# Kernel optimization log

Hardware: AMD Instinct MI355X
Metric: run time of the kernel (lower is better)

Reference implementation:

```python
import jax, jax.numpy as jnp
import numpy as np

NEG_SLOPE = 0.01  # torch F.leaky_relu default

def _lrelu(x):
    return jax.nn.leaky_relu(x, NEG_SLOPE)

def setup_inputs() -> dict:
    key = jax.random.key(0)
    ks = jax.random.split(key, 24)
    B, N, E = 512, 20000, 640000
    n_enc_1, n_enc_2, n_z = 512, 256, 64
    n_dec_2, n_dec_1, hidden = 256, 512, 256
    p = lambda k, shp, fan: jax.random.normal(k, shp, jnp.float32) * (1.0 / np.sqrt(fan))
    return {
        "data": jax.random.normal(ks[0], (B, N), jnp.float32),
        "noise": jax.random.normal(ks[1], (B, N), jnp.float32),
        "edge_index": jax.random.randint(ks[2], (2, E), 0, N, jnp.int32),
        "w_gcn": jax.random.normal(ks[3], (), jnp.float32),
        "b_gcn": jax.random.normal(ks[4], (), jnp.float32) * 0.1,
        "enc1_w": p(ks[5], (N, n_enc_1), N), "enc1_b": p(ks[6], (n_enc_1,), N),
        "enc2_w": p(ks[7], (n_enc_1, n_enc_2), n_enc_1), "enc2_b": p(ks[8], (n_enc_2,), n_enc_1),
        "enc3_w": p(ks[9], (n_enc_2, n_z), n_enc_2), "enc3_b": p(ks[10], (n_z,), n_enc_2),
        "dec1_w": p(ks[11], (n_z, n_dec_2), n_z), "dec1_b": p(ks[12], (n_dec_2,), n_z),
        "dec2_w": p(ks[13], (n_dec_2, n_dec_1), n_dec_2), "dec2_b": p(ks[14], (n_dec_1,), n_dec_2),
        "dec3_w": p(ks[15], (n_dec_1, N), n_dec_1), "dec3_b": p(ks[16], (N,), n_dec_1),
        "disc1_w": p(ks[17], (n_z, hidden), n_z), "disc1_b": p(ks[18], (hidden,), n_z),
        "disc2_w": p(ks[19], (hidden, hidden), hidden), "disc2_b": p(ks[20], (hidden,), hidden),
        "disc3_w": p(ks[21], (hidden, 1), hidden), "disc3_b": p(ks[22], (1,), hidden),
    }

def _gcn_batched(x, edge_index, w_gcn, b_gcn):
    # x: [B, N] -> GCNConv(1,1, improved=True) applied per row, vectorized.
    B, N = x.shape
    src, dst = edge_index[0], edge_index[1]
    loop = jnp.arange(N, dtype=src.dtype)
    src_a = jnp.concatenate([src, loop])
    dst_a = jnp.concatenate([dst, loop])
    # improved=True: self-loop edge weight 2.0
    ew = jnp.concatenate([jnp.ones(src.shape[0], x.dtype), jnp.full((N,), 2.0, x.dtype)])
    deg = jax.ops.segment_sum(ew, dst_a, num_segments=N)
    dinv = jnp.where(deg > 0, jax.lax.rsqrt(deg), 0.0)
    norm = dinv[src_a] * ew * dinv[dst_a]  # [E+N]
    xl = x * w_gcn                         # lin (1x1 weight, no bias)
    msgs = xl[:, src_a] * norm[None, :]    # [B, E+N]
    agg = jnp.zeros_like(x).at[:, dst_a].add(msgs)
    return agg + b_gcn

def reference(data, noise, edge_index, w_gcn, b_gcn,
              enc1_w, enc1_b, enc2_w, enc2_b, enc3_w, enc3_b,
              dec1_w, dec1_b, dec2_w, dec2_b, dec3_w, dec3_b,
              disc1_w, disc1_b, disc2_w, disc2_b, disc3_w, disc3_b):
    x = data + noise * 0.1
    gcn_out = _lrelu(_gcn_batched(x, edge_index, w_gcn, b_gcn))  # [B, N]
    h1 = _lrelu(gcn_out @ enc1_w + enc1_b)
    h2 = _lrelu(h1 @ enc2_w + enc2_b)
    z = _lrelu(h2 @ enc3_w + enc3_b)
    d1 = _lrelu(z @ dec1_w + dec1_b)
    d2 = _lrelu(d1 @ dec2_w + dec2_b)
    dec_h3 = _lrelu(d2 @ dec3_w + dec3_b)
    g1 = _lrelu(z @ disc1_w + disc1_b)
    g2 = _lrelu(g1 @ disc2_w + disc2_b)
    d = jax.nn.sigmoid(g2 @ disc3_w + disc3_b)
    return (dec_h3, z, d)
```

## Files before the change

### kernel.cpp

```cpp
#include <hip/hip_runtime.h>
#include <hip/hip_bf16.h>


#define LRELU(v) ((v) > 0.f ? (v) : 0.01f * (v))

static constexpr int Bb = 512;
static constexpr int Nn = 20000;
static constexpr int Ee = 640000;
static constexpr int KBn = 2500;
static constexpr int NPD = 20096;

typedef __attribute__((ext_vector_type(8))) short short8;
typedef __attribute__((ext_vector_type(4))) float f32x4;

__device__ __forceinline__ ushort f2bf(float f) {
  uint u = __builtin_bit_cast(uint, f);
  u = u + 0x7FFFu + ((u >> 16) & 1u);
  return (ushort)(u >> 16);
}
__device__ __forceinline__ float bfLo(uint u) {
  return __builtin_bit_cast(float, u << 16);
}
__device__ __forceinline__ float bfHi(uint u) {
  return __builtin_bit_cast(float, u & 0xffff0000u);
}

__global__ void transpose_xs_k(const float* __restrict__ a, const float* __restrict__ nz,
                               const float* __restrict__ dinv, ushort* __restrict__ xs) {
  __shared__ ushort tile[64][65];
  int c0 = blockIdx.x * 64;
  int p = blockIdx.y;
  int chunk = p >> 1;
  int sub = (p & 1) * 64;
  int rbase = p * 64;
  for (int i = threadIdx.x; i < 64 * 64; i += 256) {
    int rr = i >> 6, cc = i & 63;
    int r = rbase + rr, c = c0 + cc;
    ushort v = 0;
    if (c < Nn) {
      size_t idx = (size_t)r * Nn + c;
      v = f2bf(dinv[c] * (a[idx] + 0.1f * nz[idx]));
    }
    tile[rr][cc] = v;
  }
  __syncthreads();
  for (int i = threadIdx.x; i < 64 * 64; i += 256) {
    int cc = i >> 6, rr = i & 63;
    int c = c0 + cc;
    if (c < Nn) xs[(size_t)chunk * Nn * 128 + (size_t)c * 128 + sub + rr] = tile[rr][cc];
  }
}

__global__ void hist_check_k(const int* __restrict__ src, const int* __restrict__ dst, int E,
                             int* __restrict__ cnt, int* __restrict__ flag) {
  int i = blockIdx.x * 256 + threadIdx.x;
  if (i < E) {
    int s = src[i], d = dst[i];
    if ((unsigned)s >= (unsigned)Nn || (unsigned)d >= (unsigned)Nn) {
      atomicExch(flag, 1);
    } else {
      atomicAdd(&cnt[d], 1);
    }
  }
}

__global__ void offs_k(const int* __restrict__ cnt, int* __restrict__ offs,
                       int* __restrict__ cursor, float* __restrict__ dinv,
                       int* __restrict__ bump) {
  int i = blockIdx.x * 256 + threadIdx.x;
  int l = threadIdx.x & 63;
  int v = (i < Nn) ? cnt[i] : 0;
  int x = v;
#pragma unroll
  for (int d = 1; d < 64; d <<= 1) {
    int t = __shfl_up(x, d);
    if (l >= d) x += t;
  }
  int total = __shfl(x, 63);
  int base = 0;
  if (l == 0) base = atomicAdd(bump, total);
  base = __shfl(base, 0);
  int excl = base + x - v;
  if (i < Nn) {
    offs[i] = excl;
    cursor[i] = excl;
    dinv[i] = rsqrtf(2.0f + (float)v);
  }
}

__global__ void scatter_k(const int* __restrict__ src, const int* __restrict__ dst, int E,
                          int* __restrict__ cursor, uint* __restrict__ eOff) {
  int i = blockIdx.x * 256 + threadIdx.x;
  if (i < E) {
    int s = src[i], d = dst[i];
    if ((unsigned)s >= (unsigned)Nn || (unsigned)d >= (unsigned)Nn) return;
    int p = atomicAdd(&cursor[d], 1);
    eOff[p] = (uint)s * 256u;
  }
}

__global__ __launch_bounds__(256) void spmm_fm_k(
    const ushort* __restrict__ xs, const uint* __restrict__ eOff, const int* __restrict__ offs,
    const int* __restrict__ cnt, const float* __restrict__ dinv, const float* __restrict__ wg,
    const float* __restrict__ bg, ushort* __restrict__ gfm) {
  __shared__ uint sIdx[4][64];
  __shared__ ushort sOut[128][8];
  int bid = blockIdx.x;
  int chunk = bid & 3;
  int grp = bid >> 2;
  int wv = threadIdx.x >> 6, l = threadIdx.x & 63;
  const char* base = (const char*)(xs + (size_t)chunk * Nn * 128) + l * 4;
  float wgv = wg[0], bb = bg[0];

#pragma unroll
  for (int sub = 0; sub < 2; ++sub) {
    int n = grp * 8 + wv * 2 + sub;
    int o = offs[n], c = cnt[n];
    const uint* ep = eOff + o;
    uint su = *(const uint*)(base + (size_t)n * 256);
    float a00 = 2.0f * bfLo(su), a01 = 2.0f * bfHi(su);
    float a10 = 0.f, a11 = 0.f;

    for (int bi = 0; bi < c; bi += 64) {
      int rem = c - bi;
      if (rem > 64) rem = 64;
      sIdx[wv][l] = (l < rem) ? ep[bi + l] : 0u;
      int i = 0;
      for (; i + 16 <= rem; i += 16) {
        uint u[16];
#pragma unroll
        for (int j = 0; j < 16; ++j) u[j] = *(const uint*)(base + sIdx[wv][i + j]);
#pragma unroll
        for (int j = 0; j < 16; j += 2) {
          a00 += bfLo(u[j]);
          a01 += bfHi(u[j]);
          a10 += bfLo(u[j + 1]);
          a11 += bfHi(u[j + 1]);
        }
      }
      for (; i + 4 <= rem; i += 4) {
        uint u0 = *(const uint*)(base + sIdx[wv][i]);
        uint u1 = *(const uint*)(base + sIdx[wv][i + 1]);
        uint u2 = *(const uint*)(base + sIdx[wv][i + 2]);
        uint u3 = *(const uint*)(base + sIdx[wv][i + 3]);
        a00 += bfLo(u0);
        a01 += bfHi(u0);
        a10 += bfLo(u1);
        a11 += bfHi(u1);
        a00 += bfLo(u2);
        a01 += bfHi(u2);
        a10 += bfLo(u3);
        a11 += bfHi(u3);
      }
      for (; i < rem; ++i) {
        uint u = *(const uint*)(base + sIdx[wv][i]);
        a00 += bfLo(u);
        a01 += bfHi(u);
      }
    }

    float wdn = wgv * dinv[n];
    float v0 = wdn * (a00 + a10) + bb;
    float v1 = wdn * (a01 + a11) + bb;
    v0 = LRELU(v0);
    v1 = LRELU(v1);
    int j = wv * 2 + sub;
    sOut[2 * l][j] = f2bf(v0);
    sOut[2 * l + 1][j] = f2bf(v1);
  }
  __syncthreads();
  int row = threadIdx.x >> 1, half = threadIdx.x & 1;
  uint2 v = *(const uint2*)&sOut[row][half * 4];
  int m = chunk * 128 + row;
  *(uint2*)&gfm[((size_t)grp * 512 + m) * 8 + half * 4] = v;
}

__global__ void conv_we_k(const float* __restrict__ W, ushort* __restrict__ wef) {
  int n = blockIdx.x * 256 + threadIdx.x;
  int kb = blockIdx.y;
  ushort v[8];
#pragma unroll
  for (int j = 0; j < 8; ++j) v[j] = f2bf(W[(size_t)(8 * kb + j) * 512 + n]);
  uint4 pk;
  pk.x = (uint)v[0] | ((uint)v[1] << 16);
  pk.y = (uint)v[2] | ((uint)v[3] << 16);
  pk.z = (uint)v[4] | ((uint)v[5] << 16);
  pk.w = (uint)v[6] | ((uint)v[7] << 16);
  *(uint4*)&wef[((size_t)kb * 512 + n) * 8] = pk;
}

__global__ __launch_bounds__(256) void fmg_enc1_k(const ushort* __restrict__ gfm,
                                                  const ushort* __restrict__ wef,
                                                  float* __restrict__ C) {
  int n0 = blockIdx.x * 128, m0 = blockIdx.y * 128;
  int l = threadIdx.x & 63, w = threadIdx.x >> 6;
  int wr = w >> 1, wc = w & 1;
  int lrow = l & 15, lkg = l >> 4;
  f32x4 acc[4][4] = {};
  int ksBeg = blockIdx.z * 25, ksEnd = ksBeg + 25;

  for (int ks = ksBeg; ks < ksEnd; ++ks) {
    int kb = ks * 4 + lkg;
    short8 a[4], b[4];
#pragma unroll
    for (int mi = 0; mi < 4; ++mi) {
      int m = m0 + wr * 64 + mi * 16 + lrow;
      a[mi] = *(const short8*)&gfm[((size_t)kb * 512 + m) * 8];
    }
#pragma unroll
    for (int nj = 0; nj < 4; ++nj) {
      int n = n0 + wc * 64 + nj * 16 + lrow;
      b[nj] = *(const short8*)&wef[((size_t)kb * 512 + n) * 8];
    }
#pragma unroll
    for (int mi = 0; mi < 4; ++mi)
#pragma unroll
      for (int nj = 0; nj < 4; ++nj)
        acc[mi][nj] = __builtin_amdgcn_mfma_f32_16x16x32_bf16(a[mi], b[nj], acc[mi][nj], 0, 0, 0);
  }

#pragma unroll
  for (int mi = 0; mi < 4; ++mi)
#pragma unroll
    for (int nj = 0; nj < 4; ++nj)
#pragma unroll
      for (int r = 0; r < 4; ++r) {
        int row = m0 + wr * 64 + mi * 16 + lkg * 4 + r;
        int col = n0 + wc * 64 + nj * 16 + lrow;
        atomicAdd(&C[(size_t)row * 512 + col], acc[mi][nj][r]);
      }
}

__global__ void conv_wf_k(const float* __restrict__ W, ushort* __restrict__ wf) {
  int n = blockIdx.x * 256 + threadIdx.x;
  int kb = blockIdx.y;
  if (n >= NPD) return;
  ushort v[8];
#pragma unroll
  for (int j = 0; j < 8; ++j)
    v[j] = (n < Nn) ? f2bf(W[(size_t)(8 * kb + j) * Nn + n]) : (ushort)0;
  uint4 pk;
  pk.x = (uint)v[0] | ((uint)v[1] << 16);
  pk.y = (uint)v[2] | ((uint)v[3] << 16);
  pk.z = (uint)v[4] | ((uint)v[5] << 16);
  pk.w = (uint)v[6] | ((uint)v[7] << 16);
  *(uint4*)&wf[((size_t)kb * NPD + n) * 8] = pk;
}

__global__ __launch_bounds__(256) void fmg_dec3_k(const ushort* __restrict__ d2f,
                                                  const ushort* __restrict__ wf,
                                                  const float* __restrict__ bias,
                                                  float* __restrict__ C) {
  int n0 = blockIdx.x * 128, m0 = blockIdx.y * 128;
  int l = threadIdx.x & 63, w = threadIdx.x >> 6;
  int wr = w >> 1, wc = w & 1;
  int lrow = l & 15, lkg = l >> 4;
  f32x4 acc[4][4] = {};

#pragma unroll 4
  for (int ks = 0; ks < 16; ++ks) {
    int kb = ks * 4 + lkg;
    short8 a[4], b[4];
#pragma unroll
    for (int mi = 0; mi < 4; ++mi) {
      int m = m0 + wr * 64 + mi * 16 + lrow;
      a[mi] = *(const short8*)&d2f[((size_t)kb * 512 + m) * 8];
    }
#pragma unroll
    for (int nj = 0; nj < 4; ++nj) {
      int n = n0 + wc * 64 + nj * 16 + lrow;
      b[nj] = *(const short8*)&wf[((size_t)kb * NPD + n) * 8];
    }
#pragma unroll
    for (int mi = 0; mi < 4; ++mi)
#pragma unroll
      for (int nj = 0; nj < 4; ++nj)
        acc[mi][nj] = __builtin_amdgcn_mfma_f32_16x16x32_bf16(a[mi], b[nj], acc[mi][nj], 0, 0, 0);
  }

#pragma unroll
  for (int mi = 0; mi < 4; ++mi)
#pragma unroll
    for (int nj = 0; nj < 4; ++nj)
#pragma unroll
      for (int r = 0; r < 4; ++r) {
        int row = m0 + wr * 64 + mi * 16 + lkg * 4 + r;
        int col = n0 + wc * 64 + nj * 16 + lrow;
        if (col < Nn) {
          float v = acc[mi][nj][r] + bias[col];
          C[(size_t)row * Nn + col] = LRELU(v);
        }
      }
}

__global__ __launch_bounds__(256) void tailA_k(const float* __restrict__ h1,
                                               const float* __restrict__ c1,
                                               const float* __restrict__ W2,
                                               const float* __restrict__ c2,
                                               const float* __restrict__ W3,
                                               const float* __restrict__ c3,
                                               float* __restrict__ zbuf,
                                               float* __restrict__ out_z) {
  __shared__ float s_h1[512];
  __shared__ float s_h2[256];
  __shared__ float s_part[4][256];
  int rl = blockIdx.x;
  int t = threadIdx.x;
  int w = t >> 6, l = t & 63;

  {
    float r0 = h1[(size_t)rl * 512 + t] + c1[t];
    float r1 = h1[(size_t)rl * 512 + t + 256] + c1[t + 256];
    s_h1[t] = LRELU(r0);
    s_h1[t + 256] = LRELU(r1);
  }
  __syncthreads();

  {
    int c4 = l * 4;
    float a0 = 0.f, a1 = 0.f, a2 = 0.f, a3 = 0.f;
#pragma unroll 16
    for (int k = w * 128; k < w * 128 + 128; ++k) {
      float4 wv = *(const float4*)&W2[(size_t)k * 256 + c4];
      float x = s_h1[k];
      a0 += x * wv.x; a1 += x * wv.y; a2 += x * wv.z; a3 += x * wv.w;
    }
    float4 pv = {a0, a1, a2, a3};
    *(float4*)&s_part[w][c4] = pv;
  }
  __syncthreads();
  s_h2[t] = LRELU(s_part[0][t] + s_part[1][t] + s_part[2][t] + s_part[3][t] + c2[t]);
  __syncthreads();

  {
    int c = t >> 2, p = t & 3;
    float a = 0.f;
#pragma unroll 16
    for (int k = p * 64; k < p * 64 + 64; ++k) a += s_h2[k] * W3[(size_t)k * 64 + c];
    s_part[p][c] = a;
  }
  __syncthreads();
  if (t < 64) {
    float v = s_part[0][t] + s_part[1][t] + s_part[2][t] + s_part[3][t] + c3[t];
    v = LRELU(v);
    zbuf[(size_t)rl * 64 + t] = v;
    out_z[(size_t)rl * 64 + t] = v;
  }
}

__global__ __launch_bounds__(256) void tailB_k(
    const float* __restrict__ zbuf, const float* __restrict__ Wd1, const float* __restrict__ cd1,
    const float* __restrict__ Wd2, const float* __restrict__ cd2, const float* __restrict__ Wg1,
    const float* __restrict__ cg1, const float* __restrict__ Wg2, const float* __restrict__ cg2,
    const float* __restrict__ Wg3, const float* __restrict__ cg3, float* __restrict__ out_d,
    ushort* __restrict__ d2f) {
  __shared__ float s_z[64];
  __shared__ float s_x[256];
  __shared__ float s_part[4][256];
  __shared__ float s_g2[256];
  __shared__ float s_red[4];
  int bid = blockIdx.x;
  int rl = bid & 511;
  int t = threadIdx.x;
  int w = t >> 6, l = t & 63;

  if (t < 64) s_z[t] = zbuf[(size_t)rl * 64 + t];
  __syncthreads();

  if (bid < 512) {
    {
      float a = 0.f;
#pragma unroll
      for (int k = 0; k < 64; ++k) a += s_z[k] * Wd1[(size_t)k * 256 + t];
      s_x[t] = LRELU(a + cd1[t]);
    }
    __syncthreads();
    {
      int g = t & 127, p = t >> 7;
      int c4 = g * 4;
      float a0 = 0.f, a1 = 0.f, a2 = 0.f, a3 = 0.f;
#pragma unroll 16
      for (int k = p * 128; k < p * 128 + 128; ++k) {
        float4 wv = *(const float4*)&Wd2[(size_t)k * 512 + c4];
        float x = s_x[k];
        a0 += x * wv.x; a1 += x * wv.y; a2 += x * wv.z; a3 += x * wv.w;
      }
      float* sp = &s_part[0][0];
      float4 pv = {a0, a1, a2, a3};
      *(float4*)&sp[p * 512 + c4] = pv;
    }
    __syncthreads();
    {
      const float* sp = &s_part[0][0];
#pragma unroll
      for (int cc = 0; cc < 2; ++cc) {
        int c = t + cc * 256;
        float v = sp[c] + sp[512 + c] + cd2[c];
        v = LRELU(v);
        d2f[((size_t)(c >> 3) * 512 + rl) * 8 + (c & 7)] = f2bf(v);
      }
    }
  } else {
    {
      float a = 0.f;
#pragma unroll
      for (int k = 0; k < 64; ++k) a += s_z[k] * Wg1[(size_t)k * 256 + t];
      s_x[t] = LRELU(a + cg1[t]);
    }
    __syncthreads();
    {
      int c4 = l * 4;
      float a0 = 0.f, a1 = 0.f, a2 = 0.f, a3 = 0.f;
#pragma unroll 16
      for (int k = w * 64; k < w * 64 + 64; ++k) {
        float4 wv = *(const float4*)&Wg2[(size_t)k * 256 + c4];
        float x = s_x[k];
        a0 += x * wv.x; a1 += x * wv.y; a2 += x * wv.z; a3 += x * wv.w;
      }
      float4 pv = {a0, a1, a2, a3};
      *(float4*)&s_part[w][c4] = pv;
    }
    __syncthreads();
    s_g2[t] = LRELU(s_part[0][t] + s_part[1][t] + s_part[2][t] + s_part[3][t] + cg2[t]);
    __syncthreads();
    {
      float p = s_g2[t] * Wg3[t];
#pragma unroll
      for (int o = 32; o > 0; o >>= 1) p += __shfl_down(p, o);
      if ((t & 63) == 0) s_red[t >> 6] = p;
      __syncthreads();
      if (t == 0) {
        float s = s_red[0] + s_red[1] + s_red[2] + s_red[3] + cg3[0];
        out_d[rl] = 1.f / (1.f + __expf(-s));
      }
    }
  }
}

__global__ void sentinel_k(float* out, float val) { out[0] = val; }
__global__ void flag_sentinel_k(float* out, const int* flag) {
  if (*flag != 0) out[0] = 70000.0f;
}

extern "C" void kernel_launch(void* const* d_in, const int* in_sizes, int n_in,
                              void* d_out, int out_size, void* d_ws, size_t ws_size,
                              hipStream_t stream) {
  const float* data = (const float*)d_in[0];
  const float* noise = (const float*)d_in[1];
  const int* edge = (const int*)d_in[2];
  const int* esrc_in = edge;
  const int* edst_in = edge + Ee;
  const float* w_gcn = (const float*)d_in[3];
  const float* b_gcn = (const float*)d_in[4];
  const float* enc1_w = (const float*)d_in[5];
  const float* enc1_b = (const float*)d_in[6];
  const float* enc2_w = (const float*)d_in[7];
  const float* enc2_b = (const float*)d_in[8];
  const float* enc3_w = (const float*)d_in[9];
  const float* enc3_b = (const float*)d_in[10];
  const float* dec1_w = (const float*)d_in[11];
  const float* dec1_b = (const float*)d_in[12];
  const float* dec2_w = (const float*)d_in[13];
  const float* dec2_b = (const float*)d_in[14];
  const float* dec3_w = (const float*)d_in[15];
  const float* dec3_b = (const float*)d_in[16];
  const float* disc1_w = (const float*)d_in[17];
  const float* disc1_b = (const float*)d_in[18];
  const float* disc2_w = (const float*)d_in[19];
  const float* disc2_b = (const float*)d_in[20];
  const float* disc3_w = (const float*)d_in[21];
  const float* disc3_b = (const float*)d_in[22];

  char* w = (char*)d_ws;
  size_t o = 0;
  auto alloc = [&](size_t bytes) {
    size_t r = o;
    o = (o + bytes + 15) & ~(size_t)15;
    return r;
  };
  size_t r1 = alloc((size_t)64 * NPD * 8 * 2);
  ushort* xs = (ushort*)(w + r1);
  ushort* wef = (ushort*)(w + r1);
  ushort* wf = (ushort*)(w + r1);
  ushort* gfm = (ushort*)(w + alloc((size_t)KBn * 512 * 8 * 2));
  float* h1 = (float*)(w + alloc(512 * 512 * 4));
  ushort* d2f = (ushort*)(w + alloc((size_t)64 * 512 * 8 * 2));
  float* zbuf = (float*)(w + alloc((size_t)512 * 64 * 4));
  float* dinv = (float*)(w + alloc(Nn * 4));
  int* cnt = (int*)(w + alloc(Nn * 4));
  int* offs = (int*)(w + alloc(Nn * 4));
  int* cursor = (int*)(w + alloc(Nn * 4));
  uint* eOff = (uint*)(w + alloc(Ee * 4));
  int* flag = (int*)(w + alloc(16));

  float* outp = (float*)d_out;
  float* out_dec = outp;
  float* out_z = outp + (size_t)Bb * Nn;
  float* out_d = out_z + (size_t)Bb * 64;

  static const int expect_sizes[23] = {
      10240000, 10240000, 1280000, 1, 1,
      10240000, 512, 131072, 256, 16384, 64,
      16384, 256, 131072, 512, 10240000, 20000,
      16384, 256, 65536, 256, 256, 1};
  float host_sentinel = 0.f;
  if (n_in != 23) host_sentinel = 50000.f;
  else if (out_size != 10273280) host_sentinel = 80000.f;
  else if (ws_size < 46100000u) host_sentinel = 60000.f;
  else {
    for (int i = 0; i < 23; ++i)
      if (in_sizes[i] != expect_sizes[i]) { host_sentinel = 100000.f + 1000.f * i; break; }
  }

  hipMemsetAsync(cnt, 0, Nn * sizeof(int), stream);
  hipMemsetAsync(flag, 0, 2 * sizeof(int), stream);
  hipMemsetAsync(h1, 0, 512 * 512 * 4, stream);
  hist_check_k<<<(Ee + 255) / 256, 256, 0, stream>>>(esrc_in, edst_in, Ee, cnt, flag);
  offs_k<<<(Nn + 255) / 256, 256, 0, stream>>>(cnt, offs, cursor, dinv, flag + 1);
  scatter_k<<<(Ee + 255) / 256, 256, 0, stream>>>(esrc_in, edst_in, Ee, cursor, eOff);

  {
    dim3 g((Nn + 63) / 64, 8);
    transpose_xs_k<<<g, 256, 0, stream>>>(data, noise, dinv, xs);
  }
  spmm_fm_k<<<(Nn / 8) * 4, 256, 0, stream>>>(xs, eOff, offs, cnt, dinv, w_gcn, b_gcn, gfm);
  {
    dim3 g(2, KBn);
    conv_we_k<<<g, 256, 0, stream>>>(enc1_w, wef);
  }
  {
    dim3 g(512 / 128, 512 / 128, 25);
    fmg_enc1_k<<<g, 256, 0, stream>>>(gfm, wef, h1);
  }
  tailA_k<<<Bb, 256, 0, stream>>>(h1, enc1_b, enc2_w, enc2_b, enc3_w, enc3_b, zbuf, out_z);
  tailB_k<<<2 * Bb, 256, 0, stream>>>(zbuf, dec1_w, dec1_b, dec2_w, dec2_b, disc1_w, disc1_b,
                                      disc2_w, disc2_b, disc3_w, disc3_b, out_d, d2f);
  {
    dim3 g((NPD + 255) / 256, 64);
    conv_wf_k<<<g, 256, 0, stream>>>(dec3_w, wf);
  }
  {
    dim3 g(NPD / 128, 512 / 128);
    fmg_dec3_k<<<g, 256, 0, stream>>>(d2f, wf, dec3_b, out_dec);
  }

  flag_sentinel_k<<<1, 1, 0, stream>>>(out_dec, flag);
  if (host_sentinel != 0.f) sentinel_k<<<1, 1, 0, stream>>>(out_dec, host_sentinel);
}
```

Measured before the change: 284.5 us.

## Prefetch dec3 MFMA operands, widen enc1 split-K, vectorize SpMM index loads

The dec3 GEMM loop now software-prefetches the next K-step's A/B fragments into registers while issuing the current MFMAs, to hide global load latency. The enc1 split-K grid goes from 25 to 63 slices of 10 K-steps each, with a clamp on the last slice, to raise occupancy across CUs at the cost of more atomic or partial-sum traffic into h1. The SpMM gather reads shared-memory indices two at a time and separates index loads from data gathers to improve memory-level parallelism.

```diff
diff --git a/kernel.cpp b/kernel.cpp
--- a/kernel.cpp
+++ b/kernel.cpp
@@ -129,28 +129,37 @@
       for (; i + 16 <= rem; i += 16) {
         uint u[16];
 #pragma unroll
-        for (int j = 0; j < 16; ++j) u[j] = *(const uint*)(base + sIdx[wv][i + j]);
+        for (int j = 0; j < 8; ++j) {
+          uint2 pr = *(const uint2*)&sIdx[wv][i + 2 * j];
+          u[2 * j] = pr.x;
+          u[2 * j + 1] = pr.y;
+        }
+        uint g[16];
+#pragma unroll
+        for (int j = 0; j < 16; ++j) g[j] = *(const uint*)(base + u[j]);
 #pragma unroll
         for (int j = 0; j < 16; j += 2) {
-          a00 += bfLo(u[j]);
-          a01 += bfHi(u[j]);
-          a10 += bfLo(u[j + 1]);
-          a11 += bfHi(u[j + 1]);
+          a00 += bfLo(g[j]);
+          a01 += bfHi(g[j]);
+          a10 += bfLo(g[j + 1]);
+          a11 += bfHi(g[j + 1]);
         }
       }
       for (; i + 4 <= rem; i += 4) {
-        uint u0 = *(const uint*)(base + sIdx[wv][i]);
-        uint u1 = *(const uint*)(base + sIdx[wv][i + 1]);
-        uint u2 = *(const uint*)(base + sIdx[wv][i + 2]);
-        uint u3 = *(const uint*)(base + sIdx[wv][i + 3]);
-        a00 += bfLo(u0);
-        a01 += bfHi(u0);
-        a10 += bfLo(u1);
-        a11 += bfHi(u1);
-        a00 += bfLo(u2);
-        a01 += bfHi(u2);
-        a10 += bfLo(u3);
-        a11 += bfHi(u3);
+        uint2 p0 = *(const uint2*)&sIdx[wv][i];
+        uint2 p1 = *(const uint2*)&sIdx[wv][i + 2];
+        uint g0 = *(const uint*)(base + p0.x);
+        uint g1 = *(const uint*)(base + p0.y);
+        uint g2 = *(const uint*)(base + p1.x);
+        uint g3 = *(const uint*)(base + p1.y);
+        a00 += bfLo(g0);
+        a01 += bfHi(g0);
+        a10 += bfLo(g1);
+        a11 += bfHi(g1);
+        a00 += bfLo(g2);
+        a01 += bfHi(g2);
+        a10 += bfLo(g3);
+        a11 += bfHi(g3);
       }
       for (; i < rem; ++i) {
         uint u = *(const uint*)(base + sIdx[wv][i]);
@@ -197,7 +206,9 @@
   int wr = w >> 1, wc = w & 1;
   int lrow = l & 15, lkg = l >> 4;
   f32x4 acc[4][4] = {};
-  int ksBeg = blockIdx.z * 25, ksEnd = ksBeg + 25;
+  int ksBeg = blockIdx.z * 10;
+  int ksEnd = ksBeg + 10;
+  if (ksEnd > 625) ksEnd = 625;
 
   for (int ks = ksBeg; ks < ksEnd; ++ks) {
     int kb = ks * 4 + lkg;
@@ -257,26 +268,49 @@
   int lrow = l & 15, lkg = l >> 4;
   f32x4 acc[4][4] = {};
 
-#pragma unroll 4
+  int m_0 = m0 + wr * 64 + lrow, n_0 = n0 + wc * 64 + lrow;
+  short8 a0, a1, a2, a3, b0, b1, b2, b3;
+  short8 pa0, pa1, pa2, pa3, pb0, pb1, pb2, pb3;
+
+#define LOADF(dst_a0, dst_a1, dst_a2, dst_a3, dst_b0, dst_b1, dst_b2, dst_b3, KB_)          \
+  {                                                                                         \
+    int kb_ = (KB_);                                                                        \
+    dst_a0 = *(const short8*)&d2f[((size_t)kb_ * 512 + m_0) * 8];                           \
+    dst_a1 = *(const short8*)&d2f[((size_t)kb_ * 512 + m_0 + 16) * 8];                      \
+    dst_a2 = *(const short8*)&d2f[((size_t)kb_ * 512 + m_0 + 32) * 8];                      \
+    dst_a3 = *(const short8*)&d2f[((size_t)kb_ * 512 + m_0 + 48) * 8];                      \
+    dst_b0 = *(const short8*)&wf[((size_t)kb_ * NPD + n_0) * 8];                            \
+    dst_b1 = *(const short8*)&wf[((size_t)kb_ * NPD + n_0 + 16) * 8];                       \
+    dst_b2 = *(const short8*)&wf[((size_t)kb_ * NPD + n_0 + 32) * 8];                       \
+    dst_b3 = *(const short8*)&wf[((size_t)kb_ * NPD + n_0 + 48) * 8];                       \
+  }
+
+  LOADF(a0, a1, a2, a3, b0, b1, b2, b3, lkg);
+
+#pragma unroll 1
   for (int ks = 0; ks < 16; ++ks) {
-    int kb = ks * 4 + lkg;
-    short8 a[4], b[4];
-#pragma unroll
-    for (int mi = 0; mi < 4; ++mi) {
-      int m = m0 + wr * 64 + mi * 16 + lrow;
-      a[mi] = *(const short8*)&d2f[((size_t)kb * 512 + m) * 8];
-    }
-#pragma unroll
-    for (int nj = 0; nj < 4; ++nj) {
-      int n = n0 + wc * 64 + nj * 16 + lrow;
-      b[nj] = *(const short8*)&wf[((size_t)kb * NPD + n) * 8];
-    }
-#pragma unroll
-    for (int mi = 0; mi < 4; ++mi)
-#pragma unroll
-      for (int nj = 0; nj < 4; ++nj)
-        acc[mi][nj] = __builtin_amdgcn_mfma_f32_16x16x32_bf16(a[mi], b[nj], acc[mi][nj], 0, 0, 0);
-  }
+    if (ks + 1 < 16)
+      LOADF(pa0, pa1, pa2, pa3, pb0, pb1, pb2, pb3, (ks + 1) * 4 + lkg);
+    acc[0][0] = __builtin_amdgcn_mfma_f32_16x16x32_bf16(a0, b0, acc[0][0], 0, 0, 0);
+    acc[0][1] = __builtin_amdgcn_mfma_f32_16x16x32_bf16(a0, b1, acc[0][1], 0, 0, 0);
+    acc[0][2] = __builtin_amdgcn_mfma_f32_16x16x32_bf16(a0, b2, acc[0][2], 0, 0, 0);
+    acc[0][3] = __builtin_amdgcn_mfma_f32_16x16x32_bf16(a0, b3, acc[0][3], 0, 0, 0);
+    acc[1][0] = __builtin_amdgcn_mfma_f32_16x16x32_bf16(a1, b0, acc[1][0], 0, 0, 0);
+    acc[1][1] = __builtin_amdgcn_mfma_f32_16x16x32_bf16(a1, b1, acc[1][1], 0, 0, 0);
+    acc[1][2] = __builtin_amdgcn_mfma_f32_16x16x32_bf16(a1, b2, acc[1][2], 0, 0, 0);
+    acc[1][3] = __builtin_amdgcn_mfma_f32_16x16x32_bf16(a1, b3, acc[1][3], 0, 0, 0);
+    acc[2][0] = __builtin_amdgcn_mfma_f32_16x16x32_bf16(a2, b0, acc[2][0], 0, 0, 0);
+    acc[2][1] = __builtin_amdgcn_mfma_f32_16x16x32_bf16(a2, b1, acc[2][1], 0, 0, 0);
+    acc[2][2] = __builtin_amdgcn_mfma_f32_16x16x32_bf16(a2, b2, acc[2][2], 0, 0, 0);
+    acc[2][3] = __builtin_amdgcn_mfma_f32_16x16x32_bf16(a2, b3, acc[2][3], 0, 0, 0);
+    acc[3][0] = __builtin_amdgcn_mfma_f32_16x16x32_bf16(a3, b0, acc[3][0], 0, 0, 0);
+    acc[3][1] = __builtin_amdgcn_mfma_f32_16x16x32_bf16(a3, b1, acc[3][1], 0, 0, 0);
+    acc[3][2] = __builtin_amdgcn_mfma_f32_16x16x32_bf16(a3, b2, acc[3][2], 0, 0, 0);
+    acc[3][3] = __builtin_amdgcn_mfma_f32_16x16x32_bf16(a3, b3, acc[3][3], 0, 0, 0);
+    a0 = pa0; a1 = pa1; a2 = pa2; a3 = pa3;
+    b0 = pb0; b1 = pb1; b2 = pb2; b3 = pb3;
+  }
+#undef LOADF
 
 #pragma unroll
   for (int mi = 0; mi < 4; ++mi)
@@ -529,7 +563,7 @@
     conv_we_k<<<g, 256, 0, stream>>>(enc1_w, wef);
   }
   {
-    dim3 g(512 / 128, 512 / 128, 25);
+    dim3 g(512 / 128, 512 / 128, 63);
     fmg_enc1_k<<<g, 256, 0, stream>>>(gfm, wef, h1);
   }
   tailA_k<<<Bb, 256, 0, stream>>>(h1, enc1_b, enc2_w, enc2_b, enc3_w, enc3_b, zbuf, out_z);
```

Result: slower. 312.5 us (+9.9%).
